# Kernel optimization log

Hardware: AMD Instinct MI355X
Metric: run time of the kernel (lower is better)

Reference implementation:

```python
import jax, jax.numpy as jnp
import numpy as np

DIM = 512
HEADS = 8
DIM_HEAD = 64
INNER = HEADS * DIM_HEAD  # 512
PATCH = 64
M = 3
IN_CH = PATCH * PATCH // 2      # 2048
OUT_CH = IN_CH // 2             # 1024
B, N = 8, PATCH * PATCH // 4    # 8, 1024
SCALE = DIM_HEAD ** -0.5


def setup_inputs() -> dict:
    key = jax.random.key(0)
    ks = jax.random.split(key, 16)
    rn = lambda k, shp, s: (jax.random.normal(k, shp, dtype=jnp.float32) * s)
    inp = rn(ks[0], (B, N, DIM), 1.0)
    x = rn(ks[1], (B, N, DIM), 1.0)
    y = rn(ks[2], (B, N, DIM), 1.0)
    # Linear params (torch convention: W [out, in], y = x @ W.T + b)
    Wq = rn(ks[3], (INNER, DIM), DIM ** -0.5)
    bq = jnp.zeros((INNER,), jnp.float32)
    Wkv = rn(ks[4], (2 * INNER, DIM), DIM ** -0.5)
    bkv = jnp.zeros((2 * INNER,), jnp.float32)
    Wf = rn(ks[5], (OUT_CH + M, IN_CH + M), (IN_CH + M) ** -0.5)
    bf = jnp.zeros((OUT_CH + M,), jnp.float32)
    Wo = rn(ks[6], (DIM, INNER), INNER ** -0.5)
    bo = jnp.zeros((DIM,), jnp.float32)
    # memory tokens (xavier_normal std = sqrt(2/(m+inner)))
    std = np.sqrt(2.0 / (M + INNER))
    m_k = rn(ks[7], (1, M, INNER), std)
    m_v = rn(ks[8], (1, M, INNER), std)
    Sm_k = rn(ks[9], (1, M, INNER), std)
    Sm_v = rn(ks[10], (1, M, INNER), std)
    return dict(inp=inp, x=x, y=y, Wq=Wq, bq=bq, Wkv=Wkv, bkv=bkv,
                Wf=Wf, bf=bf, Wo=Wo, bo=bo,
                m_k=m_k, m_v=m_v, Sm_k=Sm_k, Sm_v=Sm_v)


def _split_heads(t):
    # 'b n (h d) -> b h n d'
    b, n, _ = t.shape
    return t.reshape(b, n, HEADS, DIM_HEAD).transpose(0, 2, 1, 3)


def _mem_view(p, b):
    # torch: p.expand(b, M, INNER).view(b, HEADS, M, DIM_HEAD) — raw reshape
    return jnp.broadcast_to(p, (b, M, INNER)).reshape(b, HEADS, M, DIM_HEAD)


def reference(inp, x, y, Wq, bq, Wkv, bkv, Wf, bf, Wo, bo, m_k, m_v, Sm_k, Sm_v):
    b = inp.shape[0]
    context = jnp.concatenate([x, y], axis=1)            # [b, 2n, dim]
    q = _split_heads(inp @ Wq.T + bq)                    # [b, h, n, d]
    kv = context @ Wkv.T + bkv
    k, v = jnp.split(kv, 2, axis=-1)
    k, v = _split_heads(k), _split_heads(v)              # [b, h, 2n, d]
    mk = np.sqrt(DIM_HEAD).astype(np.float32) * _mem_view(m_k, b)
    mv = np.sqrt(M).astype(np.float32) * _mem_view(m_v, b)
    k = jnp.concatenate([k, mk], axis=2)                 # [b, h, 2n+m, d]
    v = jnp.concatenate([v, mv], axis=2)
    dots = jnp.einsum('bhid,bhjd->bhij', q, k) * SCALE
    cross_attn = jax.nn.softmax(dots, axis=-1)           # [b, h, n, 2n+m]

    skv = inp @ Wkv.T + bkv
    S_k, S_v = jnp.split(skv, 2, axis=-1)
    S_k, S_v = _split_heads(S_k), _split_heads(S_v)      # [b, h, n, d]
    Smk = np.sqrt(DIM_HEAD).astype(np.float32) * _mem_view(Sm_k, b)
    Smv = np.sqrt(M).astype(np.float32) * _mem_view(Sm_v, b)
    Sk = jnp.concatenate([S_k, Smk], axis=2)             # [b, h, n+m, d]
    Sv = jnp.concatenate([S_v, Smv], axis=2)
    dots2 = jnp.einsum('bhid,bhjd->bhij', q, Sk) * SCALE
    self_attn = jax.nn.softmax(dots2, axis=-1)           # [b, h, n, n+m]

    cross_attn = cross_attn @ Wf.T + bf                  # [b, h, n, n+m]
    attn = cross_attn + self_attn
    out = jnp.einsum('bhij,bhjd->bhid', attn, Sv)        # [b, h, n, d]
    out = out.transpose(0, 2, 1, 3).reshape(b, -1, INNER)
    return out @ Wo.T + bo                               # [b, n, dim]
```

## Files before the change

kernel.cpp:

```cpp
#include <hip/hip_runtime.h>
#include <hip/hip_bf16.h>
#include <type_traits>

using bf16 = __hip_bfloat16;
typedef float f32x4 __attribute__((ext_vector_type(4)));
typedef __bf16 bf16x8_t __attribute__((ext_vector_type(8)));
typedef short  s16x8_t  __attribute__((ext_vector_type(8)));

template <typename V, typename = void> struct MfmaWorks : std::false_type {};
template <typename V>
struct MfmaWorks<V, std::void_t<decltype(__builtin_amdgcn_mfma_f32_16x16x32_bf16(
    std::declval<V>(), std::declval<V>(), std::declval<f32x4>(), 0, 0, 0))>> : std::true_type {};
using frag_t = std::conditional_t<MfmaWorks<bf16x8_t>::value, bf16x8_t, s16x8_t>;

template <typename V>
__device__ __forceinline__ f32x4 mfma_16x16x32(V a, V b, f32x4 c) {
    return __builtin_amdgcn_mfma_f32_16x16x32_bf16(a, b, c, 0, 0, 0);
}

__device__ __forceinline__ void gld_lds16(const void* g, void* l) {
    __builtin_amdgcn_global_load_lds(
        (const __attribute__((address_space(1))) unsigned int*)g,
        (__attribute__((address_space(3))) unsigned int*)l, 16, 0, 0);
}

__device__ __forceinline__ float ldin(const void* p, long i, int f32) {
    return f32 ? ((const float*)p)[i] : __bfloat162float(((const bf16*)p)[i]);
}

__global__ void detect_dtype(const void* __restrict__ inp, int* __restrict__ flag)
{
    const int t = threadIdx.x;
    int sane_cnt = 0;
#pragma unroll
    for (int s = 0; s < 4; s++) {
        float v = __bfloat162float(((const bf16*)inp)[2 * (t + 64 * s)]);
        float a = fabsf(v);
        bool sane = (a == 0.f) || (a > 9e-4f && a < 1000.f);
        unsigned long long m = __ballot(sane);
        sane_cnt += (int)__popcll(m);
    }
    if (t == 0) *flag = (sane_cnt > 128) ? 0 : 1;
}

__global__ __launch_bounds__(256)
void cvt_gen8(const void* __restrict__ src, long srcOff, bf16* __restrict__ dst,
              long nsrc, long ndst, const int* __restrict__ flag, float scale)
{
    const int f = *flag;
    const long i0 = ((long)blockIdx.x * 256 + threadIdx.x) * 8;
    if (i0 >= ndst) return;
#pragma unroll
    for (int u = 0; u < 8; u++) {
        const long i = i0 + u;
        if (i < ndst) dst[i] = __float2bfloat16(i < nsrc ? scale * ldin(src, srcOff + i, f) : 0.f);
    }
}

__global__ __launch_bounds__(256)
void cvt_weights(const void* __restrict__ Wq, const void* __restrict__ Wkv,
                 const void* __restrict__ Wo,
                 bf16* __restrict__ WqB, bf16* __restrict__ WkvB, bf16* __restrict__ WoB,
                 const int* __restrict__ flag, float qscale)
{
    const int f = *flag;
    long id = (long)blockIdx.x * 256 + threadIdx.x;
    const void* src; bf16* dst; float sc;
    if (blockIdx.x < 128)      { src = Wq;  dst = WqB;  sc = qscale; }
    else if (blockIdx.x < 384) { src = Wkv; dst = WkvB; sc = 1.f; id -= 128L * 256; }
    else                       { src = Wo;  dst = WoB;  sc = 1.f; id -= 384L * 256; }
    const long i0 = id * 8;
#pragma unroll
    for (int u = 0; u < 8; u++)
        dst[i0 + u] = __float2bfloat16(sc * ldin(src, i0 + u, f));
}

__global__ __launch_bounds__(256)
void cvt_small(const void* __restrict__ bq, const void* __restrict__ bkv,
               const void* __restrict__ bo, const void* __restrict__ mk,
               const void* __restrict__ Smk, const void* __restrict__ Smv,
               bf16* __restrict__ bqB, bf16* __restrict__ bkvB, bf16* __restrict__ boB,
               bf16* __restrict__ mkS, bf16* __restrict__ SmkS, bf16* __restrict__ SmvS,
               const int* __restrict__ flag, float qscale)
{
    const int f = *flag;
    const void* src; bf16* dst; int n; float sc;
    switch (blockIdx.x) {
        case 0:  src = bq;  dst = bqB;  n = 512;  sc = qscale;     break;
        case 1:  src = bkv; dst = bkvB; n = 1024; sc = 1.f;        break;
        case 2:  src = bo;  dst = boB;  n = 512;  sc = 1.f;        break;
        case 3:  src = mk;  dst = mkS;  n = 1536; sc = 8.f;        break;
        case 4:  src = Smk; dst = SmkS; n = 1536; sc = 8.f;        break;
        default: src = Smv; dst = SmvS; n = 1536; sc = 1.7320508f; break;
    }
    for (int i = threadIdx.x; i < n; i += 256)
        dst[i] = __float2bfloat16(sc * ldin(src, i, f));
}

__global__ __launch_bounds__(256)
void cvt_ctx8(const void* __restrict__ x, const void* __restrict__ y,
              bf16* __restrict__ ctx, const int* __restrict__ flag)
{
    const int f = *flag;
    const long i0 = ((long)blockIdx.x * 256 + threadIdx.x) * 8;
    const long r = i0 >> 9, c0 = i0 & 511;
    const long b = r >> 11, jj = r & 2047;
    const void* src = (jj < 1024) ? x : y;
    const long  soff = (jj < 1024) ? ((b * 1024 + jj) * 512 + c0)
                                   : ((b * 1024 + (jj - 1024)) * 512 + c0);
#pragma unroll
    for (int u = 0; u < 8; u++)
        ctx[i0 + u] = __float2bfloat16(ldin(src, soff + u, f));
}

__global__ __launch_bounds__(256)
void cvt_wft(const void* __restrict__ Wf, const void* __restrict__ bff,
             bf16* __restrict__ WfT, const int* __restrict__ flag)
{
    const int f = *flag;
    const long i0 = ((long)blockIdx.x * 256 + threadIdx.x) * 8;
    if (i0 >= 2176L * 1056) return;
    const long j = i0 / 1056, r0 = i0 % 1056;
    __align__(16) bf16 tmp[8];
#pragma unroll
    for (int u = 0; u < 8; u++) {
        const long r = r0 + u;
        float v = 0.f;
        if (r < 1027) {
            if (j < 2051)       v = ldin(Wf, r * 2051 + j, f);
            else if (j == 2051) v = ldin(bff, r, f);
        }
        tmp[u] = __float2bfloat16(v);
    }
    *(uint4*)(WfT + i0) = *(const uint4*)tmp;
}

__global__ __launch_bounds__(256)
void pack_k(const bf16* __restrict__ Ck, const bf16* __restrict__ mkS, bf16* __restrict__ kb)
{
    const long id = (long)blockIdx.x * 256 + threadIdx.x;
    const long bh = id / (2176 * 8);
    const long rem = id % (2176 * 8);
    const long j = rem >> 3;
    const long dg = (rem & 7) << 3;
    const long b = bh >> 3, h = bh & 7;
    bf16* dst = kb + (bh * 2176 + j) * 64 + dg;
    if (j < 2048) {
        *(uint4*)dst = *(const uint4*)(Ck + (b * 2048 + j) * 512 + h * 64 + dg);
    } else if (j < 2051) {
        *(uint4*)dst = *(const uint4*)(mkS + h * 192 + (j - 2048) * 64 + dg);
    } else {
        uint4 zz = {0, 0, 0, 0};
        *(uint4*)dst = zz;
    }
}

__global__ __launch_bounds__(256)
void pack_sk(const bf16* __restrict__ Cskv, const bf16* __restrict__ SmkS, bf16* __restrict__ Skb)
{
    const long id = (long)blockIdx.x * 256 + threadIdx.x;
    const long bh = id / (1152 * 8);
    const long rem = id % (1152 * 8);
    const long j = rem >> 3;
    const long dg = (rem & 7) << 3;
    const long b = bh >> 3, h = bh & 7;
    bf16* dst = Skb + (bh * 1152 + j) * 64 + dg;
    if (j < 1024) {
        *(uint4*)dst = *(const uint4*)(Cskv + (b * 1024 + j) * 1024 + h * 64 + dg);
    } else if (j < 1027) {
        *(uint4*)dst = *(const uint4*)(SmkS + h * 192 + (j - 1024) * 64 + dg);
    } else {
        uint4 zz = {0, 0, 0, 0};
        *(uint4*)dst = zz;
    }
}

__global__ __launch_bounds__(256)
void pack_svt(const bf16* __restrict__ Cskv, const bf16* __restrict__ SmvS,
              bf16* __restrict__ GTS, bf16* __restrict__ SvC)
{
    const long id = (long)blockIdx.x * 256 + threadIdx.x;
    const long bh = id / (128 * 132);
    const long rem = id % (128 * 132);
    const long dd = rem / 132;
    const long j0 = (rem % 132) << 3;
    const long b = bh >> 3, h = bh & 7;
    __align__(16) bf16 tmp[8];
#pragma unroll
    for (int u = 0; u < 8; u++) {
        const long j = j0 + u;
        float v = 0.f;
        if (dd < 64) {
            if (j < 1024)      v = __bfloat162float(Cskv[(b * 1024 + j) * 1024 + 512 + h * 64 + dd]);
            else if (j < 1027) v = __bfloat162float(SmvS[h * 192 + (j - 1024) * 64 + dd]);
        }
        tmp[u] = __float2bfloat16(v);
    }
    *(uint4*)(GTS + (bh * 128 + dd) * 3136 + 2080 + j0) = *(const uint4*)tmp;
    if (dd < 64)
        *(uint4*)(SvC + ((bh << 6) + dd) * 1056 + j0) = *(const uint4*)tmp;
}

__global__ __launch_bounds__(256)
void add2_cvt(const float* __restrict__ o0, const float* __restrict__ o1,
              bf16* __restrict__ outb)
{
    const long i0 = ((long)blockIdx.x * 256 + threadIdx.x) * 8;
    __align__(16) bf16 tmp[8];
#pragma unroll
    for (int u = 0; u < 8; u++)
        tmp[u] = __float2bfloat16(o0[i0 + u] + o1[i0 + u]);
    *(uint4*)(outb + i0) = *(const uint4*)tmp;
}

#define TM 128
#define TN 128
#define BK 32

template<int OMODE>
__global__ __launch_bounds__(256)
void gemm_nt(const bf16* __restrict__ A, long lda, long sAz,
             const bf16* __restrict__ B, long ldb, long sBz,
             void* __restrict__ Cv, long ldc, long sCz,
             int K,
             const bf16* __restrict__ bias,
             const bf16* __restrict__ add, long ldadd,
             int validN, int zeroN)
{
    __shared__ __align__(16) short As[TM * BK];
    __shared__ __align__(16) short Bs[TN * BK];

    const int t = threadIdx.x;
    const int wave = t >> 6;
    const int lane = t & 63;
    const int bn = blockIdx.x, bm = blockIdx.y, z = blockIdx.z;

    const bf16* Ab = A + (long)z * sAz + (long)bm * TM * lda;
    const bf16* Bb = B + (long)z * sBz + (long)bn * TN * ldb;

    const int lrow = t >> 2;
    const int lcol = (t & 3) << 3;

    const f32x4 vzero = {0.f, 0.f, 0.f, 0.f};
    f32x4 acc[4][4];
#pragma unroll
    for (int i = 0; i < 4; i++)
#pragma unroll
        for (int j = 0; j < 4; j++) acc[i][j] = vzero;

    const int wr = (wave >> 1) << 6;
    const int wc = (wave & 1) << 6;
    const int fr = lane & 15;
    const int fq = (lane >> 4) << 3;

    for (int k0 = 0; k0 < K; k0 += BK) {
        __syncthreads();
        gld_lds16(Ab + (long)lrow * lda + (k0 + lcol),        (char*)As + wave * 1024);
        gld_lds16(Ab + (long)(64 + lrow) * lda + (k0 + lcol), (char*)As + 4096 + wave * 1024);
        gld_lds16(Bb + (long)lrow * ldb + (k0 + lcol),        (char*)Bs + wave * 1024);
        gld_lds16(Bb + (long)(64 + lrow) * ldb + (k0 + lcol), (char*)Bs + 4096 + wave * 1024);
        __builtin_amdgcn_s_waitcnt(0);
        __syncthreads();

        frag_t af[4], bfr[4];
#pragma unroll
        for (int i = 0; i < 4; i++) af[i]  = *(const frag_t*)&As[(wr + i * 16 + fr) * BK + fq];
#pragma unroll
        for (int j = 0; j < 4; j++) bfr[j] = *(const frag_t*)&Bs[(wc + j * 16 + fr) * BK + fq];
#pragma unroll
        for (int i = 0; i < 4; i++)
#pragma unroll
            for (int j = 0; j < 4; j++)
                acc[i][j] = mfma_16x16x32<frag_t>(af[i], bfr[j], acc[i][j]);
    }

    const int r0 = bm * TM + wr + ((lane >> 4) << 2);
    const int c0 = bn * TN + wc + fr;
    if (OMODE == 2) {
#pragma unroll
        for (int j = 0; j < 4; j++) {
            const int c = c0 + j * 16;
            bf16* rowp = (bf16*)Cv + ((long)(c >> 6) * 128 + (c & 63)) * 3136;
#pragma unroll
            for (int i = 0; i < 4; i++) {
                const int rgb = r0 + i * 16;
                if (rgb >= zeroN) continue;
                __align__(8) bf16 t4[4];
#pragma unroll
                for (int r = 0; r < 4; r++) t4[r] = __float2bfloat16(acc[i][j][r]);
                *(uint2*)(rowp + rgb) = *(const uint2*)t4;
            }
        }
        return;
    }
#pragma unroll
    for (int j = 0; j < 4; j++) {
        const int c = c0 + j * 16;
        if (c >= zeroN) continue;
        const bool valid = c < validN;
        float bv = 0.f;
        if (valid && bias) bv = __bfloat162float(bias[c]);
#pragma unroll
        for (int i = 0; i < 4; i++)
#pragma unroll
            for (int r = 0; r < 4; r++) {
                const long rg = r0 + i * 16 + r;
                if (OMODE == 1) {
                    ((float*)Cv)[(long)z * sCz + rg * ldc + c] = acc[i][j][r] + bv;
                } else {
                    float v = 0.f;
                    if (valid) {
                        v = acc[i][j][r] + bv;
                        if (add) v += __bfloat162float(add[rg * ldadd + c]);
                    }
                    ((bf16*)Cv)[(long)z * sCz + rg * ldc + c] = __float2bfloat16(v);
                }
            }
    }
}

__global__ __launch_bounds__(256)
void attn_fused(const bf16* __restrict__ q,
                const bf16* __restrict__ kb,
                const bf16* __restrict__ Skb,
                const bf16* __restrict__ GTS,
                float* __restrict__ out0,
                float* __restrict__ out1)
{
    __shared__ __align__(16) bf16 PQ[128 * 72];
    __shared__ __align__(16) bf16 Ks[2][64 * 64];
    __shared__ __align__(16) bf16 Gs[2][64 * 64];
    __shared__ bf16 gb_lds[64];

    const int t = threadIdx.x;
    const int w = t >> 6, lane = t & 63;
    const int bh = blockIdx.x, bm = blockIdx.y;
    const int phase = blockIdx.z;
    const int b = bh >> 3, h = bh & 7;
    const int g  = lane >> 4;
    const int fr = lane & 15;
    const int fq = g << 3;

    const bf16* Qg = q + ((long)(b * 1024 + bm * 128)) * 512 + h * 64;
    {
        const int qr = t >> 3, qc0 = (t & 7) << 3;
#pragma unroll
        for (int u = 0; u < 4; u++)
            gld_lds16(Qg + (long)(u * 32 + qr) * 512 + qc0, (char*)PQ + u * 4096 + w * 1024);
    }
    if (phase == 0 && t < 64) gb_lds[t] = GTS[((long)bh * 128 + t) * 3136 + 2051];
    __builtin_amdgcn_s_waitcnt(0);
    __syncthreads();

    frag_t qf[2][2];
#pragma unroll
    for (int it = 0; it < 2; it++)
#pragma unroll
        for (int kh = 0; kh < 2; kh++)
            qf[it][kh] = *(const frag_t*)&PQ[(w * 32 + it * 16 + fr) * 64 + kh * 32 + fq];

    union { frag_t f; short s[8]; } ou;
#pragma unroll
    for (int i = 0; i < 8; i++) ou.s[i] = 0x3F80;
    const frag_t onesf = ou.f;

    const f32x4 vzero = {0.f, 0.f, 0.f, 0.f};
    bf16* Ps = PQ;
    const int rs = t >> 3, gs = t & 7;
    const int glo = gs ^ (rs & 7);

    const bf16* Kb = phase ? Skb + (long)bh * 1152 * 64 : kb + (long)bh * 2176 * 64;
    const bf16* Gb = GTS + (long)bh * 128 * 3136 + (phase ? 2080 : 0);
    const int NC = phase ? 17 : 33;
    const int valid = phase ? 1027 : 2051;

    f32x4 oacc[2][4];
    f32x4 lacc[2];
#pragma unroll
    for (int it = 0; it < 2; it++) {
        lacc[it] = vzero;
#pragma unroll
        for (int dt = 0; dt < 4; dt++) oacc[it][dt] = vzero;
    }

    __syncthreads();
    gld_lds16(Kb + (long)rs * 64 + glo * 8,          (char*)Ks[0] + w * 1024);
    gld_lds16(Kb + (long)(32 + rs) * 64 + glo * 8,   (char*)Ks[0] + 4096 + w * 1024);
    gld_lds16(Gb + (long)rs * 3136 + glo * 8,        (char*)Gs[0] + w * 1024);
    gld_lds16(Gb + (long)(32 + rs) * 3136 + glo * 8, (char*)Gs[0] + 4096 + w * 1024);

    for (int c = 0; c < NC; c++) {
        const int buf = c & 1;
        __builtin_amdgcn_s_waitcnt(0);
        __syncthreads();
        if (c + 1 < NC) {
            const bf16* Kc = Kb + (long)(c + 1) * 64 * 64;
            const bf16* Gc = Gb + (c + 1) * 64;
            gld_lds16(Kc + (long)rs * 64 + glo * 8,          (char*)Ks[buf ^ 1] + w * 1024);
            gld_lds16(Kc + (long)(32 + rs) * 64 + glo * 8,   (char*)Ks[buf ^ 1] + 4096 + w * 1024);
            gld_lds16(Gc + (long)rs * 3136 + glo * 8,        (char*)Gs[buf ^ 1] + w * 1024);
            gld_lds16(Gc + (long)(32 + rs) * 3136 + glo * 8, (char*)Gs[buf ^ 1] + 4096 + w * 1024);
        }
        const bf16* Kl = Ks[buf];
        const bf16* Gl = Gs[buf];
#pragma unroll
        for (int it = 0; it < 2; it++) {
            f32x4 s[4];
            __builtin_amdgcn_s_setprio(1);
#pragma unroll
            for (int ct = 0; ct < 4; ct++) {
                s[ct] = vzero;
#pragma unroll
                for (int kh = 0; kh < 2; kh++) {
                    const int R = ct * 16 + fr;
                    const int gph = (kh * 4 + g) ^ (R & 7);
                    const frag_t kf = *(const frag_t*)&Kl[R * 64 + gph * 8];
                    s[ct] = mfma_16x16x32<frag_t>(qf[it][kh], kf, s[ct]);
                }
            }
            __builtin_amdgcn_s_setprio(0);
            if (c == NC - 1) {
#pragma unroll
                for (int ct = 0; ct < 4; ct++) {
                    const int j = c * 64 + ct * 16 + fr;
                    if (j >= valid) {
#pragma unroll
                        for (int r = 0; r < 4; r++) s[ct][r] = -1.0e30f;
                    }
                }
            }
#pragma unroll
            for (int ct = 0; ct < 4; ct++)
#pragma unroll
                for (int r = 0; r < 4; r++)
                    Ps[(w * 32 + it * 16 + g * 4 + r) * 72 + ct * 16 + fr] =
                        __float2bfloat16(exp2f(s[ct][r]));
            __builtin_amdgcn_s_setprio(1);
#pragma unroll
            for (int kh = 0; kh < 2; kh++) {
                const frag_t pa = *(const frag_t*)&Ps[(w * 32 + it * 16 + fr) * 72 + kh * 32 + fq];
                lacc[it] = mfma_16x16x32<frag_t>(pa, onesf, lacc[it]);
#pragma unroll
                for (int dt = 0; dt < 4; dt++) {
                    const int R = dt * 16 + fr;
                    const int gph = (kh * 4 + g) ^ (R & 7);
                    const frag_t gf = *(const frag_t*)&Gl[R * 64 + gph * 8];
                    oacc[it][dt] = mfma_16x16x32<frag_t>(pa, gf, oacc[it][dt]);
                }
            }
            __builtin_amdgcn_s_setprio(0);
        }
    }

    float* Og = (phase ? out1 : out0) + ((long)(b * 1024 + bm * 128)) * 512 + h * 64;
#pragma unroll
    for (int it = 0; it < 2; it++)
#pragma unroll
        for (int r = 0; r < 4; r++) {
            const float inv = 1.f / lacc[it][r];
#pragma unroll
            for (int dt = 0; dt < 4; dt++) {
                float v = oacc[it][dt][r] * inv;
                if (phase == 0) v += __bfloat162float(gb_lds[dt * 16 + fr]);
                Og[(long)(w * 32 + it * 16 + g * 4 + r) * 512 + dt * 16 + fr] = v;
            }
        }
}

extern "C" void kernel_launch(void* const* d_in, const int* in_sizes, int n_in,
                              void* d_out, int out_size, void* d_ws, size_t ws_size,
                              hipStream_t stream)
{
    const void* inp  = d_in[0];
    const void* x    = d_in[1];
    const void* y    = d_in[2];
    const void* Wq   = d_in[3];
    const void* bq   = d_in[4];
    const void* Wkv  = d_in[5];
    const void* bkv  = d_in[6];
    const void* Wf   = d_in[7];
    const void* bff  = d_in[8];
    const void* Wo   = d_in[9];
    const void* bo   = d_in[10];
    const void* m_k  = d_in[11];
    const void* Sm_k = d_in[13];
    const void* Sm_v = d_in[14];

    char* ws = (char*)d_ws;
    int*  flag = (int*)(ws + 0);
    bf16* WqB  = (bf16*)(ws + 256);
    bf16* WkvB = (bf16*)(ws + 524544);
    bf16* WoB  = (bf16*)(ws + 1573120);
    bf16* WfT  = (bf16*)(ws + 2097408);
    bf16* bqB  = (bf16*)(ws + 6693120);
    bf16* bkvB = (bf16*)(ws + 6694144);
    bf16* boB  = (bf16*)(ws + 6696192);
    bf16* mkS  = (bf16*)(ws + 6697216);
    bf16* SmkS = (bf16*)(ws + 6700288);
    bf16* SmvS = (bf16*)(ws + 6703360);
    bf16* qb   = (bf16*)(ws + 6706432);
    bf16* kb   = (bf16*)(ws + 15095040);
    bf16* Skb  = (bf16*)(ws + 32920832);
    bf16* GTS  = (bf16*)(ws + 42358016);
    bf16* outb = (bf16*)(ws + 93738240);
    char* OV   = ws + 102126848;

    bf16* inpB = (bf16*)(OV);
    bf16* Cskv = (bf16*)(OV + 8388608);
    bf16* ctxB = (bf16*)(OV);
    bf16* Ck   = (bf16*)(OV + 16777216);
    bf16* SvC  = (bf16*)(OV + 33554432);
    float* out0f = (float*)(OV);
    float* out1f = (float*)(OV + 16777216);

    const dim3 blk(256);
    const bf16* nulb = nullptr;
    const float QS = 0.125f * 1.44269504f;

    detect_dtype<<<dim3(1), dim3(64), 0, stream>>>(inp, flag);

    cvt_weights<<<dim3(512), blk, 0, stream>>>(Wq, Wkv, Wo, WqB, WkvB, WoB, flag, QS);
    cvt_wft   <<<dim3(1122), blk, 0, stream>>>(Wf, bff, WfT, flag);
    cvt_small <<<dim3(6),    blk, 0, stream>>>(bq, bkv, bo, m_k, Sm_k, Sm_v,
                                               bqB, bkvB, boB, mkS, SmkS, SmvS, flag, QS);

    cvt_gen8<<<dim3(2048), blk, 0, stream>>>(inp, 0, inpB, 4194304, 4194304, flag, 1.f);
    gemm_nt<0><<<dim3(4, 64, 1), blk, 0, stream>>>(inpB, 512, 0, WqB, 512, 0, (void*)qb, 512, 0,
                                                   512, bqB, nulb, 0, 512, 512);
    gemm_nt<0><<<dim3(8, 64, 1), blk, 0, stream>>>(inpB, 512, 0, WkvB, 512, 0, (void*)Cskv, 1024, 0,
                                                   512, bkvB, nulb, 0, 1024, 1024);
    pack_sk <<<dim3(2304), blk, 0, stream>>>(Cskv, SmkS, Skb);
    pack_svt<<<dim3(4224), blk, 0, stream>>>(Cskv, SmvS, GTS, SvC);
    gemm_nt<2><<<dim3(32, 17, 1), blk, 0, stream>>>(WfT, 1056, 0, SvC, 1056, 0,
                                                    (void*)GTS, 0, 0,
                                                    1056, nulb, nulb, 0, 0, 2080);
    cvt_ctx8<<<dim3(4096), blk, 0, stream>>>(x, y, ctxB, flag);
    gemm_nt<0><<<dim3(4, 128, 1), blk, 0, stream>>>(ctxB, 512, 0, WkvB, 512, 0, (void*)Ck, 512, 0,
                                                    512, bkvB, nulb, 0, 512, 512);
    pack_k<<<dim3(4352), blk, 0, stream>>>(Ck, mkS, kb);

    attn_fused<<<dim3(64, 8, 2), blk, 0, stream>>>(qb, kb, Skb, GTS, out0f, out1f);
    add2_cvt<<<dim3(2048), blk, 0, stream>>>(out0f, out1f, outb);

    gemm_nt<1><<<dim3(4, 64, 1), blk, 0, stream>>>(outb, 512, 0, WoB, 512, 0, d_out, 512, 0,
                                                   512, boB, nulb, 0, 512, 512);
}
```

Before: 438.4 us.

## Shrink attention LDS with transposed scores and merge Q and self-KV GEMMs

```diff
diff --git a/kernel.cpp b/kernel.cpp
--- a/kernel.cpp
+++ b/kernel.cpp
@@ -22,6 +22,14 @@
     __builtin_amdgcn_global_load_lds(
         (const __attribute__((address_space(1))) unsigned int*)g,
         (__attribute__((address_space(3))) unsigned int*)l, 16, 0, 0);
+}
+
+__device__ __forceinline__ unsigned pack2(float lo, float hi) {
+    bf16 a = __float2bfloat16(lo), b = __float2bfloat16(hi);
+    unsigned short al, bl;
+    __builtin_memcpy(&al, &a, 2);
+    __builtin_memcpy(&bl, &b, 2);
+    return (unsigned)al | ((unsigned)bl << 16);
 }
 
 __device__ __forceinline__ float ldin(const void* p, long i, int f32) {
@@ -224,8 +232,8 @@
              void* __restrict__ Cv, long ldc, long sCz,
              int K,
              const bf16* __restrict__ bias,
-             const bf16* __restrict__ add, long ldadd,
-             int validN, int zeroN)
+             int validN, int zeroN,
+             void* __restrict__ Cv2, long ldc2, int splitN)
 {
     __shared__ __align__(16) short As[TM * BK];
     __shared__ __align__(16) short Bs[TN * BK];
@@ -300,6 +308,8 @@
         const bool valid = c < validN;
         float bv = 0.f;
         if (valid && bias) bv = __bfloat162float(bias[c]);
+        bf16* obase = (bf16*)Cv; long old = ldc; int cc = c;
+        if (OMODE == 0 && Cv2 && c >= splitN) { obase = (bf16*)Cv2; old = ldc2; cc = c - splitN; }
 #pragma unroll
         for (int i = 0; i < 4; i++)
 #pragma unroll
@@ -308,18 +318,14 @@
                 if (OMODE == 1) {
                     ((float*)Cv)[(long)z * sCz + rg * ldc + c] = acc[i][j][r] + bv;
                 } else {
-                    float v = 0.f;
-                    if (valid) {
-                        v = acc[i][j][r] + bv;
-                        if (add) v += __bfloat162float(add[rg * ldadd + c]);
-                    }
-                    ((bf16*)Cv)[(long)z * sCz + rg * ldc + c] = __float2bfloat16(v);
+                    float v = valid ? acc[i][j][r] + bv : 0.f;
+                    obase[(long)z * sCz + rg * old + cc] = __float2bfloat16(v);
                 }
             }
     }
 }
 
-__global__ __launch_bounds__(256)
+__global__ __launch_bounds__(256, 4)
 void attn_fused(const bf16* __restrict__ q,
                 const bf16* __restrict__ kb,
                 const bf16* __restrict__ Skb,
@@ -327,10 +333,9 @@
                 float* __restrict__ out0,
                 float* __restrict__ out1)
 {
-    __shared__ __align__(16) bf16 PQ[128 * 72];
     __shared__ __align__(16) bf16 Ks[2][64 * 64];
     __shared__ __align__(16) bf16 Gs[2][64 * 64];
-    __shared__ bf16 gb_lds[64];
+    __shared__ __align__(16) unsigned Psw[4][16][32];
 
     const int t = threadIdx.x;
     const int w = t >> 6, lane = t & 63;
@@ -339,16 +344,14 @@
     const int b = bh >> 3, h = bh & 7;
     const int g  = lane >> 4;
     const int fr = lane & 15;
-    const int fq = g << 3;
 
     const bf16* Qg = q + ((long)(b * 1024 + bm * 128)) * 512 + h * 64;
     {
         const int qr = t >> 3, qc0 = (t & 7) << 3;
 #pragma unroll
         for (int u = 0; u < 4; u++)
-            gld_lds16(Qg + (long)(u * 32 + qr) * 512 + qc0, (char*)PQ + u * 4096 + w * 1024);
-    }
-    if (phase == 0 && t < 64) gb_lds[t] = GTS[((long)bh * 128 + t) * 3136 + 2051];
+            gld_lds16(Qg + (long)(u * 32 + qr) * 512 + qc0, (char*)Ks + u * 4096 + w * 1024);
+    }
     __builtin_amdgcn_s_waitcnt(0);
     __syncthreads();
 
@@ -357,7 +360,8 @@
     for (int it = 0; it < 2; it++)
 #pragma unroll
         for (int kh = 0; kh < 2; kh++)
-            qf[it][kh] = *(const frag_t*)&PQ[(w * 32 + it * 16 + fr) * 64 + kh * 32 + fq];
+            qf[it][kh] = *(const frag_t*)&((const bf16*)Ks)[(w * 32 + it * 16 + fr) * 64 + kh * 32 + g * 8];
+    __syncthreads();
 
     union { frag_t f; short s[8]; } ou;
 #pragma unroll
@@ -365,7 +369,6 @@
     const frag_t onesf = ou.f;
 
     const f32x4 vzero = {0.f, 0.f, 0.f, 0.f};
-    bf16* Ps = PQ;
     const int rs = t >> 3, gs = t & 7;
     const int glo = gs ^ (rs & 7);
 
@@ -383,11 +386,13 @@
         for (int dt = 0; dt < 4; dt++) oacc[it][dt] = vzero;
     }
 
-    __syncthreads();
     gld_lds16(Kb + (long)rs * 64 + glo * 8,          (char*)Ks[0] + w * 1024);
     gld_lds16(Kb + (long)(32 + rs) * 64 + glo * 8,   (char*)Ks[0] + 4096 + w * 1024);
     gld_lds16(Gb + (long)rs * 3136 + glo * 8,        (char*)Gs[0] + w * 1024);
     gld_lds16(Gb + (long)(32 + rs) * 3136 + glo * 8, (char*)Gs[0] + 4096 + w * 1024);
+
+    unsigned* prow = &Psw[w][fr][0];
+    const int swzk = (fr & 7) << 2;
 
     for (int c = 0; c < NC; c++) {
         const int buf = c & 1;
@@ -403,55 +408,71 @@
         }
         const bf16* Kl = Ks[buf];
         const bf16* Gl = Gs[buf];
+
+        f32x4 s2[2][4];
+#pragma unroll
+        for (int it = 0; it < 2; it++)
+#pragma unroll
+            for (int ct = 0; ct < 4; ct++) s2[it][ct] = vzero;
+        __builtin_amdgcn_s_setprio(1);
+#pragma unroll
+        for (int ct = 0; ct < 4; ct++)
+#pragma unroll
+            for (int kh = 0; kh < 2; kh++) {
+                const int gph = (kh * 4 + g) ^ (fr & 7);
+                const frag_t kf = *(const frag_t*)&Kl[(ct * 16 + fr) * 64 + gph * 8];
+                s2[0][ct] = mfma_16x16x32<frag_t>(kf, qf[0][kh], s2[0][ct]);
+                s2[1][ct] = mfma_16x16x32<frag_t>(kf, qf[1][kh], s2[1][ct]);
+            }
+        __builtin_amdgcn_s_setprio(0);
+
+        if (c == NC - 1) {
+#pragma unroll
+            for (int ct = 0; ct < 4; ct++)
+#pragma unroll
+                for (int r = 0; r < 4; r++) {
+                    const int kAbs = c * 64 + ct * 16 + 4 * g + r;
+                    if (kAbs >= valid) { s2[0][ct][r] = -1.0e30f; s2[1][ct][r] = -1.0e30f; }
+                }
+        }
+
+        frag_t pa[2][2];
 #pragma unroll
         for (int it = 0; it < 2; it++) {
-            f32x4 s[4];
-            __builtin_amdgcn_s_setprio(1);
 #pragma unroll
             for (int ct = 0; ct < 4; ct++) {
-                s[ct] = vzero;
-#pragma unroll
-                for (int kh = 0; kh < 2; kh++) {
-                    const int R = ct * 16 + fr;
-                    const int gph = (kh * 4 + g) ^ (R & 7);
-                    const frag_t kf = *(const frag_t*)&Kl[R * 64 + gph * 8];
-                    s[ct] = mfma_16x16x32<frag_t>(qf[it][kh], kf, s[ct]);
-                }
+                const unsigned w0 = pack2(exp2f(s2[it][ct][0]), exp2f(s2[it][ct][1]));
+                const unsigned w1 = pack2(exp2f(s2[it][ct][2]), exp2f(s2[it][ct][3]));
+                *(uint2*)&prow[(ct * 8 + 2 * g) ^ swzk] = make_uint2(w0, w1);
             }
-            __builtin_amdgcn_s_setprio(0);
-            if (c == NC - 1) {
-#pragma unroll
-                for (int ct = 0; ct < 4; ct++) {
-                    const int j = c * 64 + ct * 16 + fr;
-                    if (j >= valid) {
-#pragma unroll
-                        for (int r = 0; r < 4; r++) s[ct][r] = -1.0e30f;
-                    }
-                }
+#pragma unroll
+            for (int kh = 0; kh < 2; kh++)
+                pa[it][kh] = *(const frag_t*)&prow[(kh * 16 + 4 * g) ^ swzk];
+        }
+
+        __builtin_amdgcn_s_setprio(1);
+#pragma unroll
+        for (int kh = 0; kh < 2; kh++) {
+            lacc[0] = mfma_16x16x32<frag_t>(pa[0][kh], onesf, lacc[0]);
+            lacc[1] = mfma_16x16x32<frag_t>(pa[1][kh], onesf, lacc[1]);
+#pragma unroll
+            for (int dt = 0; dt < 4; dt++) {
+                const int gph = (kh * 4 + g) ^ (fr & 7);
+                const frag_t gf = *(const frag_t*)&Gl[(dt * 16 + fr) * 64 + gph * 8];
+                oacc[0][dt] = mfma_16x16x32<frag_t>(pa[0][kh], gf, oacc[0][dt]);
+                oacc[1][dt] = mfma_16x16x32<frag_t>(pa[1][kh], gf, oacc[1][dt]);
             }
-#pragma unroll
-            for (int ct = 0; ct < 4; ct++)
-#pragma unroll
-                for (int r = 0; r < 4; r++)
-                    Ps[(w * 32 + it * 16 + g * 4 + r) * 72 + ct * 16 + fr] =
-                        __float2bfloat16(exp2f(s[ct][r]));
-            __builtin_amdgcn_s_setprio(1);
-#pragma unroll
-            for (int kh = 0; kh < 2; kh++) {
-                const frag_t pa = *(const frag_t*)&Ps[(w * 32 + it * 16 + fr) * 72 + kh * 32 + fq];
-                lacc[it] = mfma_16x16x32<frag_t>(pa, onesf, lacc[it]);
-#pragma unroll
-                for (int dt = 0; dt < 4; dt++) {
-                    const int R = dt * 16 + fr;
-                    const int gph = (kh * 4 + g) ^ (R & 7);
-                    const frag_t gf = *(const frag_t*)&Gl[R * 64 + gph * 8];
-                    oacc[it][dt] = mfma_16x16x32<frag_t>(pa, gf, oacc[it][dt]);
-                }
-            }
-            __builtin_amdgcn_s_setprio(0);
-        }
-    }
-
+        }
+        __builtin_amdgcn_s_setprio(0);
+    }
+
+    float gba[4] = {0.f, 0.f, 0.f, 0.f};
+    if (phase == 0) {
+        const bf16* gp = GTS + (long)bh * 128 * 3136 + 2051;
+#pragma unroll
+        for (int dt = 0; dt < 4; dt++)
+            gba[dt] = __bfloat162float(gp[(long)(dt * 16 + fr) * 3136]);
+    }
     float* Og = (phase ? out1 : out0) + ((long)(b * 1024 + bm * 128)) * 512 + h * 64;
 #pragma unroll
     for (int it = 0; it < 2; it++)
@@ -460,9 +481,8 @@
             const float inv = 1.f / lacc[it][r];
 #pragma unroll
             for (int dt = 0; dt < 4; dt++) {
-                float v = oacc[it][dt][r] * inv;
-                if (phase == 0) v += __bfloat162float(gb_lds[dt * 16 + fr]);
-                Og[(long)(w * 32 + it * 16 + g * 4 + r) * 512 + dt * 16 + fr] = v;
+                Og[(long)(w * 32 + it * 16 + g * 4 + r) * 512 + dt * 16 + fr] =
+                    oacc[it][dt][r] * inv + gba[dt];
             }
         }
 }
@@ -516,6 +536,7 @@
     const dim3 blk(256);
     const bf16* nulb = nullptr;
     const float QS = 0.125f * 1.44269504f;
+    const int NOSPLIT = 1 << 30;
 
     detect_dtype<<<dim3(1), dim3(64), 0, stream>>>(inp, flag);
 
@@ -525,23 +546,25 @@
                                                bqB, bkvB, boB, mkS, SmkS, SmvS, flag, QS);
 
     cvt_gen8<<<dim3(2048), blk, 0, stream>>>(inp, 0, inpB, 4194304, 4194304, flag, 1.f);
-    gemm_nt<0><<<dim3(4, 64, 1), blk, 0, stream>>>(inpB, 512, 0, WqB, 512, 0, (void*)qb, 512, 0,
-                                                   512, bqB, nulb, 0, 512, 512);
-    gemm_nt<0><<<dim3(8, 64, 1), blk, 0, stream>>>(inpB, 512, 0, WkvB, 512, 0, (void*)Cskv, 1024, 0,
-                                                   512, bkvB, nulb, 0, 1024, 1024);
+    gemm_nt<0><<<dim3(12, 64, 1), blk, 0, stream>>>(inpB, 512, 0, WqB, 512, 0, (void*)qb, 512, 0,
+                                                    512, bqB, 1536, 1536,
+                                                    (void*)Cskv, 1024, 512);
     pack_sk <<<dim3(2304), blk, 0, stream>>>(Cskv, SmkS, Skb);
     pack_svt<<<dim3(4224), blk, 0, stream>>>(Cskv, SmvS, GTS, SvC);
     gemm_nt<2><<<dim3(32, 17, 1), blk, 0, stream>>>(WfT, 1056, 0, SvC, 1056, 0,
                                                     (void*)GTS, 0, 0,
-                                                    1056, nulb, nulb, 0, 0, 2080);
+                                                    1056, nulb, 0, 2080,
+                                                    nullptr, 0, NOSPLIT);
     cvt_ctx8<<<dim3(4096), blk, 0, stream>>>(x, y, ctxB, flag);
     gemm_nt<0><<<dim3(4, 128, 1), blk, 0, stream>>>(ctxB, 512, 0, WkvB, 512, 0, (void*)Ck, 512, 0,
-                                                    512, bkvB, nulb, 0, 512, 512);
+                                                    512, bkvB, 512, 512,
+                                                    nullptr, 0, NOSPLIT);
     pack_k<<<dim3(4352), blk, 0, stream>>>(Ck, mkS, kb);
 
     attn_fused<<<dim3(64, 8, 2), blk, 0, stream>>>(qb, kb, Skb, GTS, out0f, out1f);
     add2_cvt<<<dim3(2048), blk, 0, stream>>>(out0f, out1f, outb);
 
     gemm_nt<1><<<dim3(4, 64, 1), blk, 0, stream>>>(outb, 512, 0, WoB, 512, 0, d_out, 512, 0,
-                                                   512, boB, nulb, 0, 512, 512);
-}
+                                                   512, boB, 512, 512,
+                                                   nullptr, 0, NOSPLIT);
+}
```

Measured after the change: 394.9 us. -9.9%, faster.
